# Performance work log

Hardware: AMD Instinct MI355X
Metric: run time of the kernel (lower is better)

## Reference

```python
import jax, jax.numpy as jnp
import numpy as np

TEMPERATURE = 0.1  # matches init kwarg


def _l2_normalize(x):
    # tf.math.l2_normalize along axis=1
    return x / jnp.sqrt(jnp.sum(x * x, axis=1, keepdims=True))


def _nearest_neighbour(p, queue):
    # brute-force top-1 retrieval: [B,D] @ [D,Q] -> argmax -> gather
    sims = p @ queue.T                      # [B, Q]
    nn = queue[jnp.argmax(sims, axis=1)]    # [B, D]
    return p + jax.lax.stop_gradient(nn - p)


def setup_inputs() -> dict:
    key = jax.random.key(0)
    k1, k2, k3 = jax.random.split(key, 3)
    B, Q, D = 4096, 32768, 128
    return {
        "projections_1": jax.random.normal(k1, (B, D), dtype=jnp.float32),
        "projections_2": jax.random.normal(k2, (B, D), dtype=jnp.float32),
        "feature_queue": _l2_normalize(jax.random.normal(k3, (Q, D), dtype=jnp.float32)),
    }


def reference(projections_1, projections_2, feature_queue):
    p1 = _l2_normalize(projections_1)
    p2 = _l2_normalize(projections_2)
    n1 = _nearest_neighbour(p1, feature_queue)
    n2 = _nearest_neighbour(p2, feature_queue)
    t = TEMPERATURE
    s_1_2_1 = (n1 @ p2.T) / t   # [B, B]
    s_1_2_2 = (p2 @ n1.T) / t
    s_2_1_1 = (n2 @ p1.T) / t
    s_2_1_2 = (p1 @ n2.T) / t
    logits = jnp.concatenate([s_1_2_1, s_1_2_2, s_2_1_1, s_2_1_2], axis=0)  # [4B, B]
    B = p1.shape[0]
    labels = jnp.tile(jnp.arange(B), 4)  # [4B]
    log_probs = jax.nn.log_softmax(logits, axis=1)
    # sparse categorical crossentropy per row (from_logits=True)
    loss = -jnp.take_along_axis(log_probs, labels[:, None], axis=1)[:, 0]
    return loss
```

## Files before the change

### kernel.cpp

```cpp
#include <hip/hip_runtime.h>
#include <math.h>


#define B_N 4096
#define D_N 128
#define NP 8192
#define NTILE 512
#define INV_T 10.0f
#define C1F (10.0f * 1.4426950408889634f)
#define C2F (16.0f * 1.4426950408889634f)
#define W_WIN 8e-3f

typedef _Float16 half8 __attribute__((ext_vector_type(8)));
typedef __fp16 fp16x2 __attribute__((ext_vector_type(2)));
typedef float f32x4 __attribute__((ext_vector_type(4)));
union H8 { half8 v; fp16x2 h2[4]; };

#define OFF_PH 0u
#define OFF_QH 2097152u
#define OFF_NH 10485760u
#define OFF_TV 12582912u
#define OFF_RMU 20971520u
#define OFF_KEY 21004288u
#define OFF_DG 21069824u
#define OFF_SP 21102592u

__device__ __forceinline__ void gload16(const void* g, void* l) {
  __builtin_amdgcn_global_load_lds((const __attribute__((address_space(1))) void*)g,
                                   (__attribute__((address_space(3))) void*)l, 16, 0, 0);
}

__device__ __forceinline__ unsigned packf(float f) {
  unsigned u = __float_as_uint(f);
  return ((int)u < 0) ? ~u : (u | 0x80000000u);
}
__device__ __forceinline__ float unpackf(unsigned p) {
  unsigned v = (p & 0x80000000u) ? (p & 0x7fffffffu) : ~p;
  return __uint_as_float(v);
}

__global__ __launch_bounds__(256) void k_prep(const float* __restrict__ in1,
                                              const float* __restrict__ in2,
                                              const float* __restrict__ queue,
                                              _Float16* __restrict__ Ph,
                                              _Float16* __restrict__ Qh,
                                              unsigned long long* __restrict__ keys,
                                              unsigned* __restrict__ rmu) {
  int bid = blockIdx.x, t = threadIdx.x;
  if (bid < 2048) {
    int i = bid * 256 + t;
    const float* s = queue + (size_t)i * 8;
    float4 x = *(const float4*)s;
    float4 y = *(const float4*)(s + 4);
    H8 h;
    h.h2[0] = __builtin_amdgcn_cvt_pkrtz(x.x, x.y);
    h.h2[1] = __builtin_amdgcn_cvt_pkrtz(x.z, x.w);
    h.h2[2] = __builtin_amdgcn_cvt_pkrtz(y.x, y.y);
    h.h2[3] = __builtin_amdgcn_cvt_pkrtz(y.z, y.w);
    *(half8*)(Qh + (size_t)i * 8) = h.v;
  } else {
    int w = t >> 6, l = t & 63;
    int g = (bid - 2048) * 4 + w;
    int view = g >> 12, row = g & (B_N - 1);
    const float* src = (view ? in2 : in1) + (size_t)row * D_N;
    float2 v = *(const float2*)(src + 2 * l);
    float ss = fmaf(v.x, v.x, v.y * v.y);
#pragma unroll
    for (int m = 1; m < 64; m <<= 1) ss += __shfl_xor(ss, m);
    float rn = 1.0f / sqrtf(ss);
    *(fp16x2*)(Ph + (size_t)g * D_N + 2 * l) = __builtin_amdgcn_cvt_pkrtz(v.x * rn, v.y * rn);
    if (l == 0) keys[g] = 0ull;
    if (l == 1) rmu[g] = 0u;
  }
}

#define STAGE128(MAT, RB, BUF)                                                 \
  {                                                                            \
    _Pragma("unroll") for (int j = 0; j < 8; ++j) {                            \
      int ch = w * 8 + j;                                                      \
      int r = (ch << 2) + l4;                                                  \
      gload16(MAT + (((RB) + r) << 7) + ((l15 ^ (r & 7)) << 3),                \
              (char*)(&sm[BUF][0]) + (ch << 10));                              \
    }                                                                          \
  }

__global__ __launch_bounds__(256, 2) void k_nn(const _Float16* __restrict__ Qh,
                                               const _Float16* __restrict__ Ph,
                                               _Float16* __restrict__ tv,
                                               unsigned* __restrict__ rmu) {
  __shared__ _Float16 sm[2][16384];
  int bid = blockIdx.x;
  int qc = (bid & 7) | ((bid >> 9) << 3);
  int pb = (bid >> 3) & 63;
  int t = threadIdx.x, l = t & 63, w = t >> 6;
  int wq = w >> 1, wp = w & 1, l15 = l & 15, l4 = l >> 4;
  half8 Pf4[4][4];
  const _Float16* pbase = Ph + (size_t)(pb * 128 + wp * 64 + l15) * D_N + l4 * 8;
#pragma unroll
  for (int tj = 0; tj < 4; ++tj)
#pragma unroll
    for (int ks = 0; ks < 4; ++ks)
      Pf4[tj][ks] = *(const half8*)(pbase + (size_t)tj * 16 * D_N + ks * 32);
  const size_t qrow0 = (size_t)qc * 2048;
  int tidb = qc * 32;
  int pcol = pb * 128 + wp * 64 + l15;
  float runm[4];
#pragma unroll
  for (int tj = 0; tj < 4; ++tj) runm[tj] = -3e38f;
  STAGE128(Qh, qrow0, 0)
#pragma unroll 1
  for (int qt = 0; qt < 16; ++qt) {
    int cur = qt & 1;
    __syncthreads();
    if (qt < 15) STAGE128(Qh, qrow0 + (qt + 1) * 128, cur ^ 1)
    const char* bb = (const char*)(&sm[cur][0]);
    f32x4 acc[4][4];
#pragma unroll
    for (int i = 0; i < 4; ++i)
#pragma unroll
      for (int j = 0; j < 4; ++j) acc[i][j] = (f32x4){0.f, 0.f, 0.f, 0.f};
#pragma unroll
    for (int ks = 0; ks < 4; ++ks) {
      half8 Qf[4];
#pragma unroll
      for (int ti = 0; ti < 4; ++ti) {
        int qloc = wq * 64 + ti * 16 + l15;
        int byteo = qloc * 256 + ((((ks << 2) + l4) ^ (qloc & 7)) << 4);
        Qf[ti] = *(const half8*)(bb + byteo);
      }
#pragma unroll
      for (int ti = 0; ti < 4; ++ti)
#pragma unroll
        for (int tj = 0; tj < 4; ++tj)
          acc[ti][tj] =
              __builtin_amdgcn_mfma_f32_16x16x32_f16(Qf[ti], Pf4[tj][ks], acc[ti][tj], 0, 0, 0);
    }
    int tid = tidb + qt * 2 + wq;
#pragma unroll
    for (int tj = 0; tj < 4; ++tj) {
      float m = acc[0][tj][0];
#pragma unroll
      for (int ti = 0; ti < 4; ++ti)
#pragma unroll
        for (int r = 0; r < 4; ++r) m = fmaxf(m, acc[ti][tj][r]);
      m = fmaxf(m, __shfl_xor(m, 16));
      m = fmaxf(m, __shfl_xor(m, 32));
      runm[tj] = fmaxf(runm[tj], m);
      if (l4 == 0) tv[(size_t)tid * NP + pcol + tj * 16] = (_Float16)m;
    }
  }
  if (l4 == 0) {
#pragma unroll
    for (int tj = 0; tj < 4; ++tj) atomicMax(rmu + pcol + tj * 16, packf(runm[tj]));
  }
}

__global__ __launch_bounds__(256) void k_rescore(const float* __restrict__ queue,
                                                 const float* __restrict__ in1,
                                                 const float* __restrict__ in2,
                                                 const _Float16* __restrict__ tv,
                                                 const unsigned* __restrict__ rmu,
                                                 unsigned long long* __restrict__ keys) {
  __shared__ float Qs[32][132];
  __shared__ unsigned short cand[NP];
  __shared__ int cnt;
  int tile = blockIdx.x, qh = blockIdx.y, t = threadIdx.x;
  if (t == 0) cnt = 0;
  __syncthreads();
  int qbase = tile * 64 + qh * 32;
#pragma unroll
  for (int j = 0; j < 4; ++j) {
    int i = j * 256 + t;
    int r = i >> 5, c = i & 31;
    *(float4*)(&Qs[r][c << 2]) = *(const float4*)(queue + ((size_t)(qbase + r) << 7) + (c << 2));
  }
  const _Float16* tvrow = tv + (size_t)tile * NP;
#pragma unroll
  for (int j = 0; j < 4; ++j) {
    int p0 = j * 2048 + t * 8;
    half8 tvv = *(const half8*)(tvrow + p0);
    uint4 u0 = *(const uint4*)(rmu + p0);
    uint4 u1 = *(const uint4*)(rmu + p0 + 4);
    unsigned uu[8] = {u0.x, u0.y, u0.z, u0.w, u1.x, u1.y, u1.z, u1.w};
#pragma unroll
    for (int k = 0; k < 8; ++k) {
      if ((float)tvv[k] >= unpackf(uu[k]) - W_WIN) {
        int pos = atomicAdd(&cnt, 1);
        cand[pos] = (unsigned short)(p0 + k);
      }
    }
  }
  __syncthreads();
  int n = cnt;
  int w = t >> 6, l = t & 63, hl = l >> 5, ll = l & 31;
  for (int ci = w * 2 + hl; ci < n; ci += 8) {
    int p = cand[ci];
    const float* prow = (p < B_N) ? (in1 + ((size_t)p << 7)) : (in2 + ((size_t)(p - B_N) << 7));
    float d = 0.f;
#pragma unroll
    for (int k = 0; k < 32; ++k) {
      float4 a = *(const float4*)(prow + (k << 2));
      float4 b = *(const float4*)(&Qs[ll][k << 2]);
      d = fmaf(a.x, b.x, d);
      d = fmaf(a.y, b.y, d);
      d = fmaf(a.z, b.z, d);
      d = fmaf(a.w, b.w, d);
    }
    int idx = qbase + ll;
#pragma unroll
    for (int m = 1; m < 32; m <<= 1) {
      float ov = __shfl_xor(d, m);
      int oi = __shfl_xor(idx, m);
      if (ov > d || (ov == d && oi < idx)) {
        d = ov;
        idx = oi;
      }
    }
    if (ll == 0) {
      unsigned long long key = ((unsigned long long)packf(d) << 32) | (unsigned)(~idx);
      atomicMax(keys + p, key);
    }
  }
}

__global__ __launch_bounds__(256) void k_gather(const float* __restrict__ queue,
                                                const float* __restrict__ in1,
                                                const float* __restrict__ in2,
                                                const unsigned long long* __restrict__ keys,
                                                _Float16* __restrict__ Nh,
                                                float* __restrict__ diag) {
  int t = threadIdx.x, w = t >> 6, l = t & 63;
  int g = blockIdx.x * 4 + w;
  int view = g >> 12, row = g & (B_N - 1);
  unsigned long long key = keys[g];
  int qidx = (int)(~(unsigned)(key & 0xffffffffull));
  const float* q = queue + (size_t)qidx * D_N;
  float2 qv = *(const float2*)(q + 2 * l);
  *(fp16x2*)(Nh + (size_t)g * D_N + 2 * l) = __builtin_amdgcn_cvt_pkrtz(qv.x, qv.y);
  const float* oth = (view ? in1 : in2) + (size_t)row * D_N;
  float2 ov = *(const float2*)(oth + 2 * l);
  float ss = fmaf(ov.x, ov.x, ov.y * ov.y);
  float d = fmaf(qv.x, ov.x, qv.y * ov.y);
#pragma unroll
  for (int m = 1; m < 64; m <<= 1) {
    ss += __shfl_xor(ss, m);
    d += __shfl_xor(d, m);
  }
  if (l == 0) diag[g] = d / sqrtf(ss);
}

__global__ __launch_bounds__(256, 2) void k_loss(const _Float16* __restrict__ Ph,
                                                 const _Float16* __restrict__ Nh,
                                                 float* __restrict__ Spart) {
  __shared__ _Float16 sm[2][16384];
  __shared__ float sred[2][2][64];
  int rb = blockIdx.x;
  int chunk = blockIdx.y;
  int pair = rb >> 5, rowblk = rb & 31;
  const size_t BDh = (size_t)B_N * D_N;
  const _Float16* A = (pair == 0) ? Nh : (pair == 1) ? (Ph + BDh) : (pair == 2) ? (Nh + BDh) : Ph;
  const _Float16* Bm = (pair == 0) ? (Ph + BDh) : (pair == 1) ? Nh : (pair == 2) ? Ph : (Nh + BDh);
  int t = threadIdx.x, l = t & 63, w = t >> 6;
  int wr = w >> 1, wc = w & 1, l15 = l & 15, l4 = l >> 4;
  half8 Af[4][4];
  const _Float16* ab = A + (size_t)(rowblk * 128 + wr * 64 + l15) * D_N + l4 * 8;
#pragma unroll
  for (int ti = 0; ti < 4; ++ti)
#pragma unroll
    for (int ks = 0; ks < 4; ++ks)
      Af[ti][ks] = *(const half8*)(ab + (size_t)ti * 16 * D_N + ks * 32);
  float S[16];
#pragma unroll
  for (int i = 0; i < 16; ++i) S[i] = 0.f;
  const size_t crow0 = (size_t)chunk * 1024;
  STAGE128(Bm, crow0, 0)
#pragma unroll 1
  for (int ct = 0; ct < 8; ++ct) {
    int cur = ct & 1;
    __syncthreads();
    if (ct < 7) STAGE128(Bm, crow0 + (ct + 1) * 128, cur ^ 1)
    const char* bbp = (const char*)(&sm[cur][0]);
    f32x4 acc[4][4];
#pragma unroll
    for (int i = 0; i < 4; ++i)
#pragma unroll
      for (int j = 0; j < 4; ++j) acc[i][j] = (f32x4){0.f, 0.f, 0.f, 0.f};
#pragma unroll
    for (int ks = 0; ks < 4; ++ks) {
      half8 Bf[4];
#pragma unroll
      for (int tj = 0; tj < 4; ++tj) {
        int bloc = wc * 64 + tj * 16 + l15;
        int byteo = bloc * 256 + ((((ks << 2) + l4) ^ (bloc & 7)) << 4);
        Bf[tj] = *(const half8*)(bbp + byteo);
      }
#pragma unroll
      for (int ti = 0; ti < 4; ++ti)
#pragma unroll
        for (int tj = 0; tj < 4; ++tj)
          acc[ti][tj] =
              __builtin_amdgcn_mfma_f32_16x16x32_f16(Af[ti][ks], Bf[tj], acc[ti][tj], 0, 0, 0);
    }
#pragma unroll
    for (int ti = 0; ti < 4; ++ti)
#pragma unroll
      for (int r = 0; r < 4; ++r) {
        float e = 0.f;
#pragma unroll
        for (int tj = 0; tj < 4; ++tj) e += exp2f(fmaf(acc[ti][tj][r], C1F, -C2F));
        S[ti * 4 + r] += e;
      }
  }
#pragma unroll
  for (int i = 0; i < 16; ++i) {
#pragma unroll
    for (int m = 1; m < 16; m <<= 1) S[i] += __shfl_xor(S[i], m);
  }
  __syncthreads();
  if (l15 == 0) {
#pragma unroll
    for (int ti = 0; ti < 4; ++ti)
#pragma unroll
      for (int r = 0; r < 4; ++r) sred[wr][wc][ti * 16 + l4 * 4 + r] = S[ti * 4 + r];
  }
  __syncthreads();
  if (t < 128) {
    int wrr = t >> 6, rl = t & 63;
    float s = sred[wrr][0][rl] + sred[wrr][1][rl];
    int row = pair * B_N + rowblk * 128 + wrr * 64 + rl;
    Spart[(size_t)row * 4 + chunk] = s;
  }
}

__global__ __launch_bounds__(256) void k_merge(const float* __restrict__ Spart,
                                               const float* __restrict__ diag,
                                               float* __restrict__ out) {
  int row = blockIdx.x * 256 + threadIdx.x;
  const float* sp = Spart + (size_t)row * 4;
  float s = sp[0] + sp[1] + sp[2] + sp[3];
  int pair = row >> 12, r = row & (B_N - 1);
  float dg = diag[(pair >> 1) * B_N + r];
  out[row] = logf(s) + 16.0f - INV_T * dg;
}

extern "C" void kernel_launch(void* const* d_in, const int* in_sizes, int n_in,
                              void* d_out, int out_size, void* d_ws, size_t ws_size,
                              hipStream_t stream) {
  const float* in1 = (const float*)d_in[0];
  const float* in2 = (const float*)d_in[1];
  const float* queue = (const float*)d_in[2];
  float* out = (float*)d_out;
  char* ws = (char*)d_ws;
  _Float16* Ph = (_Float16*)(ws + OFF_PH);
  _Float16* Qhh = (_Float16*)(ws + OFF_QH);
  _Float16* Nh = (_Float16*)(ws + OFF_NH);
  _Float16* TV = (_Float16*)(ws + OFF_TV);
  unsigned* RMU = (unsigned*)(ws + OFF_RMU);
  unsigned long long* KEY = (unsigned long long*)(ws + OFF_KEY);
  float* DG = (float*)(ws + OFF_DG);
  float* SP = (float*)(ws + OFF_SP);

  hipLaunchKernelGGL(k_prep, dim3(4096), dim3(256), 0, stream, in1, in2, queue, Ph, Qhh, KEY, RMU);
  hipLaunchKernelGGL(k_nn, dim3(1024), dim3(256), 0, stream, Qhh, Ph, TV, RMU);
  hipLaunchKernelGGL(k_rescore, dim3(512, 2), dim3(256), 0, stream, queue, in1, in2, TV, RMU, KEY);
  hipLaunchKernelGGL(k_gather, dim3(2048), dim3(256), 0, stream, queue, in1, in2, KEY, Nh, DG);
  hipLaunchKernelGGL(k_loss, dim3(128, 4), dim3(256), 0, stream, Ph, Nh, SP);
  hipLaunchKernelGGL(k_merge, dim3(64), dim3(256), 0, stream, SP, DG, out);
}
```

Measured before the change: 144.5 us.

## Exploit transpose symmetry to compute each similarity matrix once with row and column sums

```diff
diff --git a/kernel.cpp b/kernel.cpp
--- a/kernel.cpp
+++ b/kernel.cpp
@@ -24,6 +24,7 @@
 #define OFF_KEY 21004288u
 #define OFF_DG 21069824u
 #define OFF_SP 21102592u
+#define OFF_SP2 21364736u
 
 __device__ __forceinline__ void gload16(const void* g, void* l) {
   __builtin_amdgcn_global_load_lds((const __attribute__((address_space(1))) void*)g,
@@ -251,15 +252,16 @@
 
 __global__ __launch_bounds__(256, 2) void k_loss(const _Float16* __restrict__ Ph,
                                                  const _Float16* __restrict__ Nh,
-                                                 float* __restrict__ Spart) {
+                                                 float* __restrict__ Spart,
+                                                 float* __restrict__ Spart2) {
   __shared__ _Float16 sm[2][16384];
   __shared__ float sred[2][2][64];
   int rb = blockIdx.x;
   int chunk = blockIdx.y;
-  int pair = rb >> 5, rowblk = rb & 31;
+  int pi2 = rb >> 5, rowblk = rb & 31;
   const size_t BDh = (size_t)B_N * D_N;
-  const _Float16* A = (pair == 0) ? Nh : (pair == 1) ? (Ph + BDh) : (pair == 2) ? (Nh + BDh) : Ph;
-  const _Float16* Bm = (pair == 0) ? (Ph + BDh) : (pair == 1) ? Nh : (pair == 2) ? Ph : (Nh + BDh);
+  const _Float16* A = (pi2 == 0) ? Nh : (Nh + BDh);
+  const _Float16* Bm = (pi2 == 0) ? (Ph + BDh) : Ph;
   int t = threadIdx.x, l = t & 63, w = t >> 6;
   int wr = w >> 1, wc = w & 1, l15 = l & 15, l4 = l >> 4;
   half8 Af[4][4];
@@ -272,6 +274,7 @@
   float S[16];
 #pragma unroll
   for (int i = 0; i < 16; ++i) S[i] = 0.f;
+  float* sp2 = Spart2 + (((size_t)pi2 * 64 + rowblk * 2 + wr) << 12);
   const size_t crow0 = (size_t)chunk * 1024;
   STAGE128(Bm, crow0, 0)
 #pragma unroll 1
@@ -302,14 +305,23 @@
               __builtin_amdgcn_mfma_f32_16x16x32_f16(Af[ti][ks], Bf[tj], acc[ti][tj], 0, 0, 0);
     }
 #pragma unroll
-    for (int ti = 0; ti < 4; ++ti)
-#pragma unroll
-      for (int r = 0; r < 4; ++r) {
-        float e = 0.f;
-#pragma unroll
-        for (int tj = 0; tj < 4; ++tj) e += exp2f(fmaf(acc[ti][tj][r], C1F, -C2F));
-        S[ti * 4 + r] += e;
-      }
+    for (int tj = 0; tj < 4; ++tj) {
+      float csum = 0.f;
+#pragma unroll
+      for (int ti = 0; ti < 4; ++ti)
+#pragma unroll
+        for (int r = 0; r < 4; ++r) {
+          float e = exp2f(fmaf(acc[ti][tj][r], C1F, -C2F));
+          S[ti * 4 + r] += e;
+          csum += e;
+        }
+      csum += __shfl_xor(csum, 16);
+      csum += __shfl_xor(csum, 32);
+      if (l4 == 0) {
+        int col = chunk * 1024 + ct * 128 + wc * 64 + tj * 16 + l15;
+        sp2[col] = csum;
+      }
+    }
   }
 #pragma unroll
   for (int i = 0; i < 16; ++i) {
@@ -327,18 +339,27 @@
   if (t < 128) {
     int wrr = t >> 6, rl = t & 63;
     float s = sred[wrr][0][rl] + sred[wrr][1][rl];
-    int row = pair * B_N + rowblk * 128 + wrr * 64 + rl;
+    int row = (pi2 * 2) * B_N + rowblk * 128 + wrr * 64 + rl;
     Spart[(size_t)row * 4 + chunk] = s;
   }
 }
 
 __global__ __launch_bounds__(256) void k_merge(const float* __restrict__ Spart,
+                                               const float* __restrict__ Spart2,
                                                const float* __restrict__ diag,
                                                float* __restrict__ out) {
   int row = blockIdx.x * 256 + threadIdx.x;
-  const float* sp = Spart + (size_t)row * 4;
-  float s = sp[0] + sp[1] + sp[2] + sp[3];
   int pair = row >> 12, r = row & (B_N - 1);
+  float s;
+  if ((pair & 1) == 0) {
+    const float* sp = Spart + (size_t)row * 4;
+    s = sp[0] + sp[1] + sp[2] + sp[3];
+  } else {
+    const float* c = Spart2 + (((size_t)(pair >> 1) * 64) << 12) + r;
+    s = 0.f;
+#pragma unroll
+    for (int k = 0; k < 64; ++k) s += c[(size_t)k << 12];
+  }
   float dg = diag[(pair >> 1) * B_N + r];
   out[row] = logf(s) + 16.0f - INV_T * dg;
 }
@@ -359,11 +380,12 @@
   unsigned long long* KEY = (unsigned long long*)(ws + OFF_KEY);
   float* DG = (float*)(ws + OFF_DG);
   float* SP = (float*)(ws + OFF_SP);
+  float* SP2 = (float*)(ws + OFF_SP2);
 
   hipLaunchKernelGGL(k_prep, dim3(4096), dim3(256), 0, stream, in1, in2, queue, Ph, Qhh, KEY, RMU);
   hipLaunchKernelGGL(k_nn, dim3(1024), dim3(256), 0, stream, Qhh, Ph, TV, RMU);
   hipLaunchKernelGGL(k_rescore, dim3(512, 2), dim3(256), 0, stream, queue, in1, in2, TV, RMU, KEY);
   hipLaunchKernelGGL(k_gather, dim3(2048), dim3(256), 0, stream, queue, in1, in2, KEY, Nh, DG);
-  hipLaunchKernelGGL(k_loss, dim3(128, 4), dim3(256), 0, stream, Ph, Nh, SP);
-  hipLaunchKernelGGL(k_merge, dim3(64), dim3(256), 0, stream, SP, DG, out);
-}
+  hipLaunchKernelGGL(k_loss, dim3(64, 4), dim3(256), 0, stream, Ph, Nh, SP, SP2);
+  hipLaunchKernelGGL(k_merge, dim3(64), dim3(256), 0, stream, SP, SP2, DG, out);
+}
```

Measured after the change: 157.4 us. 1.09x slower.

## Widen k_nn P tile to 256 columns per block, halving grid and Q staging

Applied to the files above, without the earlier changes.

```diff
diff --git a/kernel.cpp b/kernel.cpp
--- a/kernel.cpp
+++ b/kernel.cpp
@@ -90,12 +90,12 @@
                                                unsigned* __restrict__ rmu) {
   __shared__ _Float16 sm[2][16384];
   int bid = blockIdx.x;
-  int qc = (bid & 7) | ((bid >> 9) << 3);
-  int pb = (bid >> 3) & 63;
+  int qc = (bid & 7) | ((bid >> 8) << 3);
+  int pb = (bid >> 3) & 31;
   int t = threadIdx.x, l = t & 63, w = t >> 6;
-  int wq = w >> 1, wp = w & 1, l15 = l & 15, l4 = l >> 4;
+  int l15 = l & 15, l4 = l >> 4;
   half8 Pf4[4][4];
-  const _Float16* pbase = Ph + (size_t)(pb * 128 + wp * 64 + l15) * D_N + l4 * 8;
+  const _Float16* pbase = Ph + (size_t)(pb * 256 + w * 64 + l15) * D_N + l4 * 8;
 #pragma unroll
   for (int tj = 0; tj < 4; ++tj)
 #pragma unroll
@@ -103,7 +103,7 @@
       Pf4[tj][ks] = *(const half8*)(pbase + (size_t)tj * 16 * D_N + ks * 32);
   const size_t qrow0 = (size_t)qc * 2048;
   int tidb = qc * 32;
-  int pcol = pb * 128 + wp * 64 + l15;
+  int pcol = pb * 256 + w * 64 + l15;
   float runm[4];
 #pragma unroll
   for (int tj = 0; tj < 4; ++tj) runm[tj] = -3e38f;
@@ -114,39 +114,44 @@
     __syncthreads();
     if (qt < 15) STAGE128(Qh, qrow0 + (qt + 1) * 128, cur ^ 1)
     const char* bb = (const char*)(&sm[cur][0]);
-    f32x4 acc[4][4];
-#pragma unroll
-    for (int i = 0; i < 4; ++i)
+    f32x4 acc[8][4];
+#pragma unroll
+    for (int i = 0; i < 8; ++i)
 #pragma unroll
       for (int j = 0; j < 4; ++j) acc[i][j] = (f32x4){0.f, 0.f, 0.f, 0.f};
 #pragma unroll
     for (int ks = 0; ks < 4; ++ks) {
-      half8 Qf[4];
-#pragma unroll
-      for (int ti = 0; ti < 4; ++ti) {
-        int qloc = wq * 64 + ti * 16 + l15;
+#pragma unroll
+      for (int ti = 0; ti < 8; ++ti) {
+        int qloc = ti * 16 + l15;
         int byteo = qloc * 256 + ((((ks << 2) + l4) ^ (qloc & 7)) << 4);
-        Qf[ti] = *(const half8*)(bb + byteo);
-      }
-#pragma unroll
-      for (int ti = 0; ti < 4; ++ti)
+        half8 Qf = *(const half8*)(bb + byteo);
 #pragma unroll
         for (int tj = 0; tj < 4; ++tj)
           acc[ti][tj] =
-              __builtin_amdgcn_mfma_f32_16x16x32_f16(Qf[ti], Pf4[tj][ks], acc[ti][tj], 0, 0, 0);
-    }
-    int tid = tidb + qt * 2 + wq;
+              __builtin_amdgcn_mfma_f32_16x16x32_f16(Qf, Pf4[tj][ks], acc[ti][tj], 0, 0, 0);
+      }
+    }
+    int tid = tidb + qt * 2;
 #pragma unroll
     for (int tj = 0; tj < 4; ++tj) {
-      float m = acc[0][tj][0];
+      float mA = acc[0][tj][0], mB = acc[4][tj][0];
 #pragma unroll
       for (int ti = 0; ti < 4; ++ti)
 #pragma unroll
-        for (int r = 0; r < 4; ++r) m = fmaxf(m, acc[ti][tj][r]);
-      m = fmaxf(m, __shfl_xor(m, 16));
-      m = fmaxf(m, __shfl_xor(m, 32));
-      runm[tj] = fmaxf(runm[tj], m);
-      if (l4 == 0) tv[(size_t)tid * NP + pcol + tj * 16] = (_Float16)m;
+        for (int r = 0; r < 4; ++r) {
+          mA = fmaxf(mA, acc[ti][tj][r]);
+          mB = fmaxf(mB, acc[ti + 4][tj][r]);
+        }
+      mA = fmaxf(mA, __shfl_xor(mA, 16));
+      mA = fmaxf(mA, __shfl_xor(mA, 32));
+      mB = fmaxf(mB, __shfl_xor(mB, 16));
+      mB = fmaxf(mB, __shfl_xor(mB, 32));
+      runm[tj] = fmaxf(runm[tj], fmaxf(mA, mB));
+      if (l4 == 0) {
+        tv[(size_t)tid * NP + pcol + tj * 16] = (_Float16)mA;
+        tv[(size_t)(tid + 1) * NP + pcol + tj * 16] = (_Float16)mB;
+      }
     }
   }
   if (l4 == 0) {
@@ -361,7 +366,7 @@
   float* SP = (float*)(ws + OFF_SP);
 
   hipLaunchKernelGGL(k_prep, dim3(4096), dim3(256), 0, stream, in1, in2, queue, Ph, Qhh, KEY, RMU);
-  hipLaunchKernelGGL(k_nn, dim3(1024), dim3(256), 0, stream, Qhh, Ph, TV, RMU);
+  hipLaunchKernelGGL(k_nn, dim3(512), dim3(256), 0, stream, Qhh, Ph, TV, RMU);
   hipLaunchKernelGGL(k_rescore, dim3(512, 2), dim3(256), 0, stream, queue, in1, in2, TV, RMU, KEY);
   hipLaunchKernelGGL(k_gather, dim3(2048), dim3(256), 0, stream, queue, in1, in2, KEY, Nh, DG);
   hipLaunchKernelGGL(k_loss, dim3(128, 4), dim3(256), 0, stream, Ph, Nh, SP);
```

Result: slower. 157.6 us (+9.0%).
